# Performance work log

Measured on AMD Instinct MI355X. Metric: run time of the kernel, lower is better.

Reference implementation:

```python
import jax, jax.numpy as jnp
import numpy as np
import math

B, H, L, D = 2, 16, 2048, 128

def setup_inputs() -> dict:
    key = jax.random.key(0)
    kq, kk, kv, km = jax.random.split(key, 4)
    q = jax.random.normal(kq, (B, H, L, D), dtype=jnp.float32)
    k = jax.random.normal(kk, (B, H, L, D), dtype=jnp.float32)
    v = jax.random.normal(kv, (B, H, L, D), dtype=jnp.float32)
    mask = jax.random.randint(km, (B, 1, L, L), 0, 2, dtype=jnp.int32)
    return {"q": q, "k": k, "v": v, "mask": mask}

def reference(q, k, v, mask):
    d_tensor = q.shape[-1]
    # ReLU applied to V before attention (the custom twist)
    v = jax.nn.relu(v)
    # score = q @ k^T / sqrt(d)  -> [B,H,L,L]
    score = jnp.einsum('bhqd,bhkd->bhqk', q, k) / math.sqrt(d_tensor)
    score = jnp.where(mask == 0, jnp.float32(-10000.0), score)
    attn = jax.nn.softmax(score, axis=-1)
    # result = attn @ relu(v) -> [B,H,L,D]
    return jnp.einsum('bhqk,bhkd->bhqd', attn, v)
```

## Files before the change

### kernel.cpp

```cpp
#include <hip/hip_runtime.h>
#include <hip/hip_bf16.h>
#include <math.h>

typedef __attribute__((ext_vector_type(8)))  short short8;
typedef __attribute__((ext_vector_type(16))) float f32x16;

#define Bc    2
#define Hc    16
#define Lc    2048
#define Dc    128
#define QBLK  128
#define KBLK  64
#define LOG2E 1.4426950408889634f
#define SCALE 0.08838834764831845f
#define SCL2  (SCALE * LOG2E)

#define KB_OFF   0u
#define KB_BYTES (32u * 2048u * 128u * 2u)
#define VT_OFF   (KB_OFF + KB_BYTES)
#define VT_BYTES (32u * 2048u * 128u * 2u)
#define MB_OFF   (VT_OFF + VT_BYTES)
#define MB_BYTES (2u * 2048u * 32u * 8u)

__device__ __forceinline__ unsigned pk2(float a, float b) {
    unsigned short ua = __builtin_bit_cast(unsigned short, __float2bfloat16(a));
    unsigned short ub = __builtin_bit_cast(unsigned short, __float2bfloat16(b));
    return (unsigned)ua | ((unsigned)ub << 16);
}
__device__ __forceinline__ unsigned short bf16b(float a) {
    return __builtin_bit_cast(unsigned short, __float2bfloat16(a));
}
__device__ __forceinline__ void gload_lds16(const void* g, void* l) {
    __builtin_amdgcn_global_load_lds(
        (const __attribute__((address_space(1))) unsigned int*)g,
        (__attribute__((address_space(3))) unsigned int*)l, 16, 0, 0);
}
__device__ __forceinline__ unsigned cvtpk(float lo, float hi) {
    unsigned r;
    asm("v_cvt_pk_bf16_f32 %0, %1, %2" : "=v"(r) : "v"(lo), "v"(hi));
    return r;
}

__global__ void prepass_kernel(const float* __restrict__ k, const float* __restrict__ v,
                               const int* __restrict__ mask,
                               unsigned short* __restrict__ kb, unsigned short* __restrict__ vt,
                               unsigned long long* __restrict__ mb) {
    __shared__ float t[32][33];
    int bid = blockIdx.x;
    int tid = threadIdx.x;
    if (bid < 4096) {
        size_t base = ((size_t)bid * 256 + tid) * 8;
        float4 f0 = *(const float4*)(k + base);
        float4 f1 = *(const float4*)(k + base + 4);
        uint4 w;
        w.x = pk2(f0.x, f0.y); w.y = pk2(f0.z, f0.w);
        w.z = pk2(f1.x, f1.y); w.w = pk2(f1.z, f1.w);
        *(uint4*)(kb + base) = w;
    } else if (bid < 12288) {
        int b2 = bid - 4096;
        int bh = b2 >> 8, rem = b2 & 255;
        int l0 = (rem >> 2) * 32, d0 = (rem & 3) * 32;
        int tx = tid & 31, ty = tid >> 5;
        const float* src = v + (size_t)bh * Lc * Dc;
        unsigned short* dst = vt + (size_t)bh * Dc * Lc;
        #pragma unroll
        for (int i = 0; i < 4; ++i) {
            int row = ty * 4 + i;
            t[row][tx] = fmaxf(src[(size_t)(l0 + row) * Dc + d0 + tx], 0.f);
        }
        __syncthreads();
        #pragma unroll
        for (int i = 0; i < 4; ++i) {
            int drow = ty * 4 + i;
            dst[(size_t)(d0 + drow) * Lc + l0 + tx] = bf16b(t[tx][drow]);
        }
    } else {
        int m = bid - 12288;
        int wv = tid >> 6, lane = tid & 63;
        #pragma unroll
        for (int i = 0; i < 16; ++i) {
            int wid = m * 64 + wv * 16 + i;
            int b = wid >> 16, l = (wid >> 5) & 2047, ktw = wid & 31;
            int mm = mask[(((size_t)(b * 2048 + l)) << 11) + ktw * 64 + lane];
            unsigned long long bal = __ballot(mm != 0);
            if (lane == 0) mb[(((size_t)(b * 32 + ktw)) << 11) + l] = bal;
        }
    }
}

__global__ __launch_bounds__(256, 2) void rev_attn_kernel(
    const float* __restrict__ q,
    const unsigned short* __restrict__ kb,
    const unsigned short* __restrict__ vt,
    const unsigned long long* __restrict__ mb,
    float* __restrict__ out)
{
    __shared__ __align__(16) char smem[65536];

    const int tid  = threadIdx.x;
    const int w    = tid >> 6;
    const int lane = tid & 63;
    const int l31  = lane & 31;
    const int hi   = lane >> 5;
    const int bh   = blockIdx.y;
    const int b    = bh >> 4;
    const int qb   = blockIdx.x * QBLK + w * 32;
    const int qrow = qb + l31;

    const float*              qp = q  + (size_t)bh * Lc * Dc;
    const unsigned short*     kp = kb + (size_t)bh * Lc * Dc;
    const unsigned short*     vp = vt + (size_t)bh * Dc * Lc;
    const unsigned long long* mp = mb + ((size_t)b << 16);
    float*                    op = out + (size_t)bh * Lc * Dc;

    short8 qf[8];
    {
        const float* qr0 = qp + (size_t)qrow * Dc + hi * 8;
        #pragma unroll
        for (int c = 0; c < 8; ++c) {
            const float* src = qr0 + c * 16;
            #pragma unroll
            for (int j = 0; j < 8; ++j)
                qf[c][j] = (short)bf16b(src[j] * SCL2);
        }
    }

    unsigned koff[8], voff[8];
    #pragma unroll
    for (int c = 0; c < 8; ++c)
        koff[c] = (unsigned)(l31 * 256 + ((((c << 1) | hi) ^ (l31 & 15)) << 4));
    #pragma unroll
    for (int hs = 0; hs < 2; ++hs)
        #pragma unroll
        for (int ks = 0; ks < 4; ++ks)
            voff[hs * 4 + ks] = (unsigned)(l31 * 256 +
                ((((hs << 3) | (ks << 1) | hi) ^ (l31 & 15)) << 4));

    const unsigned short *kp0, *kp1, *kp2, *kp3, *vp0, *vp1, *vp2, *vp3;
    {
        #define INITP(P, KP, VP) {                                   \
            int l   = (P) * 256 + tid;                               \
            int row = l >> 4, cl = l & 15;                           \
            int s_  = cl ^ (row & 15);                               \
            KP = kp + (size_t)row * Dc + s_ * 8;                     \
            int ds_ = row + ((s_ >> 3) << 6);                        \
            int ko_ = (s_ & 7) * 8;                                  \
            VP = vp + (size_t)ds_ * Lc + ko_;                        \
        }
        INITP(0, kp0, vp0) INITP(1, kp1, vp1) INITP(2, kp2, vp2) INITP(3, kp3, vp3)
        #undef INITP
    }

    f32x16 o0 = (f32x16)0.f, o1 = (f32x16)0.f, o2 = (f32x16)0.f, o3 = (f32x16)0.f;
    f32x16 lacc = (f32x16)0.f;
    short8 ones;
    #pragma unroll
    for (int j = 0; j < 8; ++j) ones[j] = (short)0x3F80;

    #define STAGE(buf) do {                                                        \
        char* Kdst = smem + (buf) * 16384;                                         \
        char* Vdst = smem + 32768 + (buf) * 16384;                                 \
        gload_lds16(kp0, Kdst + tid * 16);                                         \
        gload_lds16(vp0, Vdst + tid * 16);                                         \
        gload_lds16(kp1, Kdst + 4096 + tid * 16);                                  \
        gload_lds16(vp1, Vdst + 4096 + tid * 16);                                  \
        gload_lds16(kp2, Kdst + 8192 + tid * 16);                                  \
        gload_lds16(vp2, Vdst + 8192 + tid * 16);                                  \
        gload_lds16(kp3, Kdst + 12288 + tid * 16);                                 \
        gload_lds16(vp3, Vdst + 12288 + tid * 16);                                 \
        kp0 += KBLK * Dc; kp1 += KBLK * Dc; kp2 += KBLK * Dc; kp3 += KBLK * Dc;    \
        vp0 += KBLK;      vp1 += KBLK;      vp2 += KBLK;      vp3 += KBLK;         \
    } while (0)

    #define MK_SLICE(PA, SV, J0, CS0, MREG) do {                                   \
        float e0 = ((MREG >> (CS0 + 0)) & 1u)  ? __builtin_amdgcn_exp2f(SV[J0 + 0]) : 0.f; \
        float e1 = ((MREG >> (CS0 + 1)) & 1u)  ? __builtin_amdgcn_exp2f(SV[J0 + 1]) : 0.f; \
        float e2 = ((MREG >> (CS0 + 2)) & 1u)  ? __builtin_amdgcn_exp2f(SV[J0 + 2]) : 0.f; \
        float e3 = ((MREG >> (CS0 + 3)) & 1u)  ? __builtin_amdgcn_exp2f(SV[J0 + 3]) : 0.f; \
        float e4 = ((MREG >> (CS0 + 8)) & 1u)  ? __builtin_amdgcn_exp2f(SV[J0 + 4]) : 0.f; \
        float e5 = ((MREG >> (CS0 + 9)) & 1u)  ? __builtin_amdgcn_exp2f(SV[J0 + 5]) : 0.f; \
        float e6 = ((MREG >> (CS0 + 10)) & 1u) ? __builtin_amdgcn_exp2f(SV[J0 + 6]) : 0.f; \
        float e7 = ((MREG >> (CS0 + 11)) & 1u) ? __builtin_amdgcn_exp2f(SV[J0 + 7]) : 0.f; \
        unsigned a_ = cvtpk(e0, e1), a2_ = cvtpk(e2, e3);                          \
        unsigned b_ = cvtpk(e4, e5), b2_ = cvtpk(e6, e7);                          \
        asm volatile("v_permlane32_swap_b32 %0, %1" : "+v"(a_),  "+v"(b_));        \
        asm volatile("v_permlane32_swap_b32 %0, %1" : "+v"(a2_), "+v"(b2_));       \
        union { unsigned u[4]; short8 v8; } tu_;                                   \
        tu_.u[0] = a_; tu_.u[1] = a2_; tu_.u[2] = b_; tu_.u[3] = b2_;              \
        PA = tu_.v8;                                                               \
    } while (0)

    #define PV_SLICE(PA, KS) do {                                                  \
        __builtin_amdgcn_s_setprio(1);                                             \
        lacc = __builtin_amdgcn_mfma_f32_32x32x16_bf16(ones, PA, lacc, 0, 0, 0);   \
        short8 vfa = *(const short8*)(Vb + voff[KS]);                              \
        o0 = __builtin_amdgcn_mfma_f32_32x32x16_bf16(vfa, PA, o0, 0, 0, 0);        \
        short8 vfb = *(const short8*)(Vb + voff[KS] + 8192);                       \
        o1 = __builtin_amdgcn_mfma_f32_32x32x16_bf16(vfb, PA, o1, 0, 0, 0);        \
        short8 vfc = *(const short8*)(Vb + voff[4 + KS]);                          \
        o2 = __builtin_amdgcn_mfma_f32_32x32x16_bf16(vfc, PA, o2, 0, 0, 0);        \
        short8 vfd = *(const short8*)(Vb + voff[4 + KS] + 8192);                   \
        o3 = __builtin_amdgcn_mfma_f32_32x32x16_bf16(vfd, PA, o3, 0, 0, 0);        \
        __builtin_amdgcn_s_setprio(0);                                             \
    } while (0)

    int cur = 0;
    STAGE(0);
    asm volatile("s_waitcnt vmcnt(0)" ::: "memory");
    __builtin_amdgcn_s_barrier();
    __builtin_amdgcn_sched_barrier(0);

    for (int kt = 0; kt < Lc; kt += KBLK) {
        STAGE(cur ^ 1);
        unsigned long long mw = mp[((size_t)(kt >> 6) << 11) + qrow];

        asm volatile("s_waitcnt vmcnt(9)" ::: "memory");
        __builtin_amdgcn_s_barrier();
        __builtin_amdgcn_sched_barrier(0);

        const char* Kb = smem + cur * 16384;
        const char* Vb = smem + 32768 + cur * 16384;

        f32x16 s0 = (f32x16)0.f, s1 = (f32x16)0.f;
        __builtin_amdgcn_s_setprio(1);
        #pragma unroll
        for (int c = 0; c < 8; ++c) {
            short8 kf0 = *(const short8*)(Kb + koff[c]);
            s0 = __builtin_amdgcn_mfma_f32_32x32x16_bf16(kf0, qf[c], s0, 0, 0, 0);
            short8 kf1 = *(const short8*)(Kb + koff[c] + 8192);
            s1 = __builtin_amdgcn_mfma_f32_32x32x16_bf16(kf1, qf[c], s1, 0, 0, 0);
        }
        __builtin_amdgcn_s_setprio(0);

        unsigned m0 = ((unsigned)(mw & 0xffffffffull)) >> (4 * hi);
        unsigned m1 = ((unsigned)(mw >> 32)) >> (4 * hi);

        short8 pa;
        MK_SLICE(pa, s0, 0, 0,  m0);  PV_SLICE(pa, 0);
        MK_SLICE(pa, s0, 8, 16, m0);  PV_SLICE(pa, 1);
        MK_SLICE(pa, s1, 0, 0,  m1);  PV_SLICE(pa, 2);
        MK_SLICE(pa, s1, 8, 16, m1);  PV_SLICE(pa, 3);

        asm volatile("" ::: "memory");
        __builtin_amdgcn_s_barrier();
        __builtin_amdgcn_sched_barrier(0);
        cur ^= 1;
    }

    __syncthreads();
    float inv = 1.0f / lacc[0];
    float* scr = (float*)(smem + w * 4608);
    const int qq = lane >> 1;
    const int dh = (lane & 1) * 16;
    #pragma unroll
    for (int dt = 0; dt < 4; ++dt) {
        const f32x16& oo = (dt == 0) ? o0 : (dt == 1) ? o1 : (dt == 2) ? o2 : o3;
        #pragma unroll
        for (int r = 0; r < 16; ++r) {
            int drow = (r & 3) + 8 * (r >> 2) + 4 * hi;
            scr[drow * 36 + l31] = oo[r] * inv;
        }
        asm volatile("s_waitcnt lgkmcnt(0)" ::: "memory");
        __builtin_amdgcn_sched_barrier(0);
        float t[16];
        #pragma unroll
        for (int c2 = 0; c2 < 16; ++c2)
            t[c2] = scr[(dh + c2) * 36 + qq];
        asm volatile("s_waitcnt lgkmcnt(0)" ::: "memory");
        __builtin_amdgcn_sched_barrier(0);
        float* od = op + (size_t)(qb + qq) * Dc + dt * 32 + dh;
        #pragma unroll
        for (int c2 = 0; c2 < 4; ++c2) {
            float4 f4; f4.x = t[c2*4]; f4.y = t[c2*4+1]; f4.z = t[c2*4+2]; f4.w = t[c2*4+3];
            *(float4*)(od + c2 * 4) = f4;
        }
    }
}

extern "C" void kernel_launch(void* const* d_in, const int* in_sizes, int n_in,
                              void* d_out, int out_size, void* d_ws, size_t ws_size,
                              hipStream_t stream) {
    const float* q    = (const float*)d_in[0];
    const float* k    = (const float*)d_in[1];
    const float* v    = (const float*)d_in[2];
    const int*   mask = (const int*)d_in[3];
    float*       out  = (float*)d_out;

    char* ws = (char*)d_ws;
    unsigned short*     kb  = (unsigned short*)(ws + KB_OFF);
    unsigned short*     vt  = (unsigned short*)(ws + VT_OFF);
    unsigned long long* mbp = (unsigned long long*)(ws + MB_OFF);

    hipLaunchKernelGGL(prepass_kernel, dim3(14336), dim3(256), 0, stream, k, v, mask, kb, vt, mbp);
    hipLaunchKernelGGL(rev_attn_kernel, dim3(Lc / QBLK, Bc * Hc), dim3(256), 0, stream,
                       q, kb, vt, mbp, out);
}
```

Measured before the change: 112.3 us.

## Software-pipeline QK^T of next tile with softmax-PV of previous tile

Restructures the main loop so each iteration computes QK^T for the current K tile while running exp/PV on the previous tile's scores. K and V loads are staged separately, so the V buffer stays live one stage longer. The ones-vector MFMA for the row sum is replaced by a scalar running sum of the exponentials plus a cross-half shuffle at the end, which saves one MFMA per slice. In exchange, two score accumulators raise register pressure and the prologue/epilogue code becomes more complex.

```diff
diff --git a/kernel.cpp b/kernel.cpp
--- a/kernel.cpp
+++ b/kernel.cpp
@@ -152,24 +152,39 @@
     }
 
     f32x16 o0 = (f32x16)0.f, o1 = (f32x16)0.f, o2 = (f32x16)0.f, o3 = (f32x16)0.f;
-    f32x16 lacc = (f32x16)0.f;
-    short8 ones;
-    #pragma unroll
-    for (int j = 0; j < 8; ++j) ones[j] = (short)0x3F80;
-
-    #define STAGE(buf) do {                                                        \
-        char* Kdst = smem + (buf) * 16384;                                         \
-        char* Vdst = smem + 32768 + (buf) * 16384;                                 \
-        gload_lds16(kp0, Kdst + tid * 16);                                         \
-        gload_lds16(vp0, Vdst + tid * 16);                                         \
-        gload_lds16(kp1, Kdst + 4096 + tid * 16);                                  \
-        gload_lds16(vp1, Vdst + 4096 + tid * 16);                                  \
-        gload_lds16(kp2, Kdst + 8192 + tid * 16);                                  \
-        gload_lds16(vp2, Vdst + 8192 + tid * 16);                                  \
-        gload_lds16(kp3, Kdst + 12288 + tid * 16);                                 \
-        gload_lds16(vp3, Vdst + 12288 + tid * 16);                                 \
+    f32x16 sA0, sA1, sB0, sB1;
+    float lrun = 0.f;
+    unsigned long long mw_prev, mw_cur;
+
+    #define STAGE_K(buf) do {                                                      \
+        char* Kd = smem + (buf) * 16384;                                           \
+        gload_lds16(kp0, Kd + tid * 16);                                           \
+        gload_lds16(kp1, Kd + 4096 + tid * 16);                                    \
+        gload_lds16(kp2, Kd + 8192 + tid * 16);                                    \
+        gload_lds16(kp3, Kd + 12288 + tid * 16);                                   \
         kp0 += KBLK * Dc; kp1 += KBLK * Dc; kp2 += KBLK * Dc; kp3 += KBLK * Dc;    \
-        vp0 += KBLK;      vp1 += KBLK;      vp2 += KBLK;      vp3 += KBLK;         \
+    } while (0)
+    #define STAGE_V(buf) do {                                                      \
+        char* Vd = smem + 32768 + (buf) * 16384;                                   \
+        gload_lds16(vp0, Vd + tid * 16);                                           \
+        gload_lds16(vp1, Vd + 4096 + tid * 16);                                    \
+        gload_lds16(vp2, Vd + 8192 + tid * 16);                                    \
+        gload_lds16(vp3, Vd + 12288 + tid * 16);                                   \
+        vp0 += KBLK; vp1 += KBLK; vp2 += KBLK; vp3 += KBLK;                        \
+    } while (0)
+
+    #define QKT(S0v, S1v, KBASE) do {                                              \
+        S0v = (f32x16)0.f; S1v = (f32x16)0.f;                                      \
+        const char* Kb_ = smem + (KBASE);                                          \
+        __builtin_amdgcn_s_setprio(1);                                             \
+        _Pragma("unroll")                                                          \
+        for (int c = 0; c < 8; ++c) {                                              \
+            short8 kf0 = *(const short8*)(Kb_ + koff[c]);                          \
+            S0v = __builtin_amdgcn_mfma_f32_32x32x16_bf16(kf0, qf[c], S0v, 0, 0, 0); \
+            short8 kf1 = *(const short8*)(Kb_ + koff[c] + 8192);                   \
+            S1v = __builtin_amdgcn_mfma_f32_32x32x16_bf16(kf1, qf[c], S1v, 0, 0, 0); \
+        }                                                                          \
+        __builtin_amdgcn_s_setprio(0);                                             \
     } while (0)
 
     #define MK_SLICE(PA, SV, J0, CS0, MREG) do {                                   \
@@ -181,6 +196,7 @@
         float e5 = ((MREG >> (CS0 + 9)) & 1u)  ? __builtin_amdgcn_exp2f(SV[J0 + 5]) : 0.f; \
         float e6 = ((MREG >> (CS0 + 10)) & 1u) ? __builtin_amdgcn_exp2f(SV[J0 + 6]) : 0.f; \
         float e7 = ((MREG >> (CS0 + 11)) & 1u) ? __builtin_amdgcn_exp2f(SV[J0 + 7]) : 0.f; \
+        lrun += ((e0 + e1) + (e2 + e3)) + ((e4 + e5) + (e6 + e7));                 \
         unsigned a_ = cvtpk(e0, e1), a2_ = cvtpk(e2, e3);                          \
         unsigned b_ = cvtpk(e4, e5), b2_ = cvtpk(e6, e7);                          \
         asm volatile("v_permlane32_swap_b32 %0, %1" : "+v"(a_),  "+v"(b_));        \
@@ -190,65 +206,71 @@
         PA = tu_.v8;                                                               \
     } while (0)
 
-    #define PV_SLICE(PA, KS) do {                                                  \
+    #define PV_SLICE(PA, KS, VBASE) do {                                           \
         __builtin_amdgcn_s_setprio(1);                                             \
-        lacc = __builtin_amdgcn_mfma_f32_32x32x16_bf16(ones, PA, lacc, 0, 0, 0);   \
-        short8 vfa = *(const short8*)(Vb + voff[KS]);                              \
+        short8 vfa = *(const short8*)(smem + (VBASE) + voff[KS]);                  \
         o0 = __builtin_amdgcn_mfma_f32_32x32x16_bf16(vfa, PA, o0, 0, 0, 0);        \
-        short8 vfb = *(const short8*)(Vb + voff[KS] + 8192);                       \
+        short8 vfb = *(const short8*)(smem + (VBASE) + voff[KS] + 8192);           \
         o1 = __builtin_amdgcn_mfma_f32_32x32x16_bf16(vfb, PA, o1, 0, 0, 0);        \
-        short8 vfc = *(const short8*)(Vb + voff[4 + KS]);                          \
+        short8 vfc = *(const short8*)(smem + (VBASE) + voff[4 + KS]);              \
         o2 = __builtin_amdgcn_mfma_f32_32x32x16_bf16(vfc, PA, o2, 0, 0, 0);        \
-        short8 vfd = *(const short8*)(Vb + voff[4 + KS] + 8192);                   \
+        short8 vfd = *(const short8*)(smem + (VBASE) + voff[4 + KS] + 8192);       \
         o3 = __builtin_amdgcn_mfma_f32_32x32x16_bf16(vfd, PA, o3, 0, 0, 0);        \
         __builtin_amdgcn_s_setprio(0);                                             \
     } while (0)
 
-    int cur = 0;
-    STAGE(0);
+    #define FINISH(S0v, S1v, MW, VBASE) do {                                       \
+        unsigned m0_ = ((unsigned)((MW) & 0xffffffffull)) >> (4 * hi);             \
+        unsigned m1_ = ((unsigned)((MW) >> 32)) >> (4 * hi);                       \
+        short8 pa;                                                                 \
+        MK_SLICE(pa, S0v, 0, 0,  m0_);  PV_SLICE(pa, 0, VBASE);                    \
+        MK_SLICE(pa, S0v, 8, 16, m0_);  PV_SLICE(pa, 1, VBASE);                    \
+        MK_SLICE(pa, S1v, 0, 0,  m1_);  PV_SLICE(pa, 2, VBASE);                    \
+        MK_SLICE(pa, S1v, 8, 16, m1_);  PV_SLICE(pa, 3, VBASE);                    \
+    } while (0)
+
+    #define BODY(T, P, SC0, SC1, SP0, SP1, MWC, MWP, LAST) do {                    \
+        STAGE_K((P) ^ 1);                                                          \
+        MWC = mp[((size_t)(T) << 11) + qrow];                                      \
+        asm volatile("s_waitcnt vmcnt(9)" ::: "memory");                           \
+        __builtin_amdgcn_s_barrier();                                              \
+        __builtin_amdgcn_sched_barrier(0);                                         \
+        QKT(SC0, SC1, (P) * 16384);                                                \
+        FINISH(SP0, SP1, MWP, 32768 + ((P) ^ 1) * 16384);                          \
+        asm volatile("" ::: "memory");                                             \
+        __builtin_amdgcn_s_barrier();                                              \
+        __builtin_amdgcn_sched_barrier(0);                                         \
+        if (!(LAST)) STAGE_V((P) ^ 1);                                             \
+    } while (0)
+
+    STAGE_K(0);
+    STAGE_V(0);
+    mw_prev = mp[qrow];
+    STAGE_K(1);
+    STAGE_V(1);
+    asm volatile("s_waitcnt vmcnt(13)" ::: "memory");
+    __builtin_amdgcn_s_barrier();
+    __builtin_amdgcn_sched_barrier(0);
+    QKT(sB0, sB1, 0);
+    asm volatile("" ::: "memory");
+    __builtin_amdgcn_s_barrier();
+    __builtin_amdgcn_sched_barrier(0);
+
+    #pragma unroll 1
+    for (int t = 1; t < 31; t += 2) {
+        BODY(t,     1, sA0, sA1, sB0, sB1, mw_cur,  mw_prev, 0);
+        BODY(t + 1, 0, sB0, sB1, sA0, sA1, mw_prev, mw_cur,  0);
+    }
+    BODY(31, 1, sA0, sA1, sB0, sB1, mw_cur, mw_prev, 1);
+
     asm volatile("s_waitcnt vmcnt(0)" ::: "memory");
     __builtin_amdgcn_s_barrier();
     __builtin_amdgcn_sched_barrier(0);
-
-    for (int kt = 0; kt < Lc; kt += KBLK) {
-        STAGE(cur ^ 1);
-        unsigned long long mw = mp[((size_t)(kt >> 6) << 11) + qrow];
-
-        asm volatile("s_waitcnt vmcnt(9)" ::: "memory");
-        __builtin_amdgcn_s_barrier();
-        __builtin_amdgcn_sched_barrier(0);
-
-        const char* Kb = smem + cur * 16384;
-        const char* Vb = smem + 32768 + cur * 16384;
-
-        f32x16 s0 = (f32x16)0.f, s1 = (f32x16)0.f;
-        __builtin_amdgcn_s_setprio(1);
-        #pragma unroll
-        for (int c = 0; c < 8; ++c) {
-            short8 kf0 = *(const short8*)(Kb + koff[c]);
-            s0 = __builtin_amdgcn_mfma_f32_32x32x16_bf16(kf0, qf[c], s0, 0, 0, 0);
-            short8 kf1 = *(const short8*)(Kb + koff[c] + 8192);
-            s1 = __builtin_amdgcn_mfma_f32_32x32x16_bf16(kf1, qf[c], s1, 0, 0, 0);
-        }
-        __builtin_amdgcn_s_setprio(0);
-
-        unsigned m0 = ((unsigned)(mw & 0xffffffffull)) >> (4 * hi);
-        unsigned m1 = ((unsigned)(mw >> 32)) >> (4 * hi);
-
-        short8 pa;
-        MK_SLICE(pa, s0, 0, 0,  m0);  PV_SLICE(pa, 0);
-        MK_SLICE(pa, s0, 8, 16, m0);  PV_SLICE(pa, 1);
-        MK_SLICE(pa, s1, 0, 0,  m1);  PV_SLICE(pa, 2);
-        MK_SLICE(pa, s1, 8, 16, m1);  PV_SLICE(pa, 3);
-
-        asm volatile("" ::: "memory");
-        __builtin_amdgcn_s_barrier();
-        __builtin_amdgcn_sched_barrier(0);
-        cur ^= 1;
-    }
+    FINISH(sA0, sA1, mw_cur, 32768 + 16384);
 
     __syncthreads();
-    float inv = 1.0f / lacc[0];
+    lrun += __shfl_xor(lrun, 32);
+    float inv = 1.0f / lrun;
     float* scr = (float*)(smem + w * 4608);
     const int qq = lane >> 1;
     const int dh = (lane & 1) * 16;
@@ -262,16 +284,16 @@
         }
         asm volatile("s_waitcnt lgkmcnt(0)" ::: "memory");
         __builtin_amdgcn_sched_barrier(0);
-        float t[16];
+        float t2[16];
         #pragma unroll
         for (int c2 = 0; c2 < 16; ++c2)
-            t[c2] = scr[(dh + c2) * 36 + qq];
+            t2[c2] = scr[(dh + c2) * 36 + qq];
         asm volatile("s_waitcnt lgkmcnt(0)" ::: "memory");
         __builtin_amdgcn_sched_barrier(0);
         float* od = op + (size_t)(qb + qq) * Dc + dt * 32 + dh;
         #pragma unroll
         for (int c2 = 0; c2 < 4; ++c2) {
-            float4 f4; f4.x = t[c2*4]; f4.y = t[c2*4+1]; f4.z = t[c2*4+2]; f4.w = t[c2*4+3];
+            float4 f4; f4.x = t2[c2*4]; f4.y = t2[c2*4+1]; f4.z = t2[c2*4+2]; f4.w = t2[c2*4+3];
             *(float4*)(od + c2 * 4) = f4;
         }
     }
```

New measurement: 344.2 us. 3.07x slower.
